# Performance work log

Hardware: AMD Instinct MI355X
Metric: run time of the kernel (lower is better)

The kernel has to match this reference:

```python
import jax, jax.numpy as jnp
import numpy as np

N_NODES = 50000
N_EDGES = 800000
IN_CH = 128
HID_CH = 128
OUT_CH = 10
NUM_GRAPHS = 128


def setup_inputs() -> dict:
    key = jax.random.key(0)
    ks = jax.random.split(key, 10)
    x = jax.random.normal(ks[0], (N_NODES, IN_CH), dtype=jnp.float32)
    edge_index = jax.random.randint(ks[1], (2, N_EDGES), 0, N_NODES, dtype=jnp.int64)
    batch = jnp.sort(jax.random.randint(ks[2], (N_NODES,), 0, NUM_GRAPHS, dtype=jnp.int64))
    s1 = 1.0 / np.sqrt(IN_CH)
    s2 = 1.0 / np.sqrt(HID_CH)
    W1 = jax.random.uniform(ks[3], (IN_CH, HID_CH), jnp.float32, -s1, s1)
    b1 = jnp.zeros((HID_CH,), jnp.float32)
    W2 = jax.random.uniform(ks[4], (HID_CH, HID_CH), jnp.float32, -s2, s2)
    b2 = jnp.zeros((HID_CH,), jnp.float32)
    Wc = jax.random.uniform(ks[5], (HID_CH, OUT_CH), jnp.float32, -s2, s2)
    bc = jax.random.uniform(ks[6], (OUT_CH,), jnp.float32, -s2, s2)
    return {"x": x, "edge_index": edge_index, "batch": batch,
            "W1": W1, "b1": b1, "W2": W2, "b2": b2, "Wc": Wc, "bc": bc}


def _gcn_norm(edge_index, num_nodes):
    # add self-loops, compute symmetric normalization deg^-1/2[src]*deg^-1/2[dst]
    loop = jnp.arange(num_nodes, dtype=edge_index.dtype)
    src = jnp.concatenate([edge_index[0], loop])
    dst = jnp.concatenate([edge_index[1], loop])
    deg = jax.ops.segment_sum(jnp.ones_like(dst, dtype=jnp.float32), dst,
                              num_segments=num_nodes)
    dinv = jnp.where(deg > 0, jax.lax.rsqrt(deg), 0.0)
    norm = dinv[src] * dinv[dst]
    return src, dst, norm


def _gcn_conv(h, src, dst, norm, W, b, num_nodes):
    h = h @ W                                    # [N, out]
    msg = h[src] * norm[:, None]                 # [E+N, out] gather + scale
    agg = jax.ops.segment_sum(msg, dst, num_segments=num_nodes)
    return agg + b


def reference(x, edge_index, batch, W1, b1, W2, b2, Wc, bc):
    n = x.shape[0]
    src, dst, norm = _gcn_norm(edge_index, n)
    h = jax.nn.relu(_gcn_conv(x, src, dst, norm, W1, b1, n))
    h = jax.nn.relu(_gcn_conv(h, src, dst, norm, W2, b2, n))
    # global mean pool over graphs
    sums = jax.ops.segment_sum(h, batch, num_segments=NUM_GRAPHS)
    cnts = jax.ops.segment_sum(jnp.ones((n,), jnp.float32), batch,
                               num_segments=NUM_GRAPHS)
    pooled = sums / jnp.maximum(cnts, 1.0)[:, None]
    # dropout is identity in eval mode
    return pooled @ Wc + bc
```

## Files before the change

### kernel.cpp

```cpp
#include <hip/hip_runtime.h>

#define N_NODES 50000
#define N_EDGES 800000
#define CH 128
#define NOUT 10
#define NUM_GRAPHS 128
#define POOL_CHUNK 50
#define GR 64
#define GEMM_BLOCKS ((N_NODES + GR - 1) / GR)
#define FILL_SEGS 128
#define FILL_CHUNK (N_EDGES / FILL_SEGS)
#define DST_RANGE (N_NODES / 8)
#define DEG_CAP 64

typedef __attribute__((ext_vector_type(8))) short bf16x8;
typedef __attribute__((ext_vector_type(4))) float f32x4;

union FragU { uint4 u; bf16x8 s; };

__device__ __forceinline__ unsigned pack_bf16(float a, float b) {
    unsigned ua = __float_as_uint(a), ub = __float_as_uint(b);
    ua += 0x7fffu + ((ua >> 16) & 1u);
    ub += 0x7fffu + ((ub >> 16) & 1u);
    return (ua >> 16) | (ub & 0xffff0000u);
}

__device__ __forceinline__ unsigned short cvt_bf16(float v) {
    unsigned u = __float_as_uint(v);
    u += 0x7fffu + ((u >> 16) & 1u);
    return (unsigned short)(u >> 16);
}

__global__ __launch_bounds__(256) void k_prep(const float* __restrict__ W1,
                                              const float* __restrict__ W2,
                                              unsigned short* __restrict__ Wb1,
                                              unsigned short* __restrict__ Wb2,
                                              int* __restrict__ fill_pos,
                                              float* __restrict__ psum) {
    if (blockIdx.x < 2) {
        const float* W = blockIdx.x ? W2 : W1;
        unsigned short* Wb = blockIdx.x ? Wb2 : Wb1;
        for (int i = threadIdx.x; i < CH * CH; i += 256) {
            int k = i >> 7, n = i & 127;
            Wb[((((k >> 3) << 7) + n) << 3) + (k & 7)] = cvt_bf16(W[i]);
        }
    } else if (blockIdx.x < 198) {
        int idx = (blockIdx.x - 2) * 256 + threadIdx.x;
        if (idx < N_NODES) fill_pos[idx] = 0;
    } else {
        psum[(blockIdx.x - 198) * 256 + threadIdx.x] = 0.f;
    }
}

template <bool SCALE>
__device__ __forceinline__ void gemm_body9(const float* __restrict__ X,
                                           const unsigned short* __restrict__ Wb,
                                           unsigned short* __restrict__ Yb,
                                           const int* __restrict__ cnt,
                                           int bid) {
    const int tid = threadIdx.x;
    const int w = tid >> 6;
    const int lane = tid & 63;
    const int m = lane & 15;
    const int quad = lane >> 4;
    const int row0 = bid * GR + w * 16;

    int row_a = row0 + m;
    if (row_a > N_NODES - 1) row_a = N_NODES - 1;
    const float4* Xr = (const float4*)(X + (size_t)row_a * CH) + quad * 2;

    f32x4 acc[8];
    #pragma unroll
    for (int ct = 0; ct < 8; ++ct) acc[ct] = (f32x4){0.f, 0.f, 0.f, 0.f};

    const uint4* Wq = (const uint4*)Wb;
    #pragma unroll
    for (int ks = 0; ks < 4; ++ks) {
        float4 a0 = Xr[ks * 8];
        float4 a1 = Xr[ks * 8 + 1];
        FragU af;
        af.u.x = pack_bf16(a0.x, a0.y);
        af.u.y = pack_bf16(a0.z, a0.w);
        af.u.z = pack_bf16(a1.x, a1.y);
        af.u.w = pack_bf16(a1.z, a1.w);
        const int kg = ks * 4 + quad;
        #pragma unroll
        for (int ct = 0; ct < 8; ++ct) {
            FragU bfu;
            bfu.u = Wq[kg * 128 + ct * 16 + m];
            acc[ct] = __builtin_amdgcn_mfma_f32_16x16x32_bf16(af.s, bfu.s, acc[ct], 0, 0, 0);
        }
    }

    #pragma unroll
    for (int r = 0; r < 4; ++r) {
        int row = row0 + quad * 4 + r;
        if (row < N_NODES) {
            float dv = SCALE ? rsqrtf((float)(cnt[row] + 1)) : 1.0f;
            unsigned short* yrow = Yb + (size_t)row * CH + m;
            #pragma unroll
            for (int ct = 0; ct < 8; ++ct)
                yrow[ct * 16] = cvt_bf16(SCALE ? acc[ct][r] * dv : acc[ct][r]);
        }
    }
}

__global__ __launch_bounds__(256) void k_gemm_fill(const float* __restrict__ X,
                                                   const unsigned short* __restrict__ Wb,
                                                   unsigned short* __restrict__ Yb,
                                                   const int* __restrict__ src,
                                                   const int* __restrict__ dst,
                                                   int* __restrict__ fill_pos,
                                                   int* __restrict__ csr_src) {
    if (blockIdx.x < GEMM_BLOCKS) {
        gemm_body9<false>(X, Wb, Yb, nullptr, blockIdx.x);
    } else {
        const int b = blockIdx.x - GEMM_BLOCKS;
        const int rng = b & 7;
        const int seg = b >> 3;
        const int lo = rng * DST_RANGE, hi = lo + DST_RANGE;
        const int base = seg * FILL_CHUNK;
        for (int it = 0; it < FILL_CHUNK; it += 256) {
            int e = base + it + threadIdx.x;
            if (it + (int)threadIdx.x < FILL_CHUNK) {
                int d = dst[e];
                if (d >= lo && d < hi) {
                    int slot = atomicAdd(&fill_pos[d], 1);
                    if (slot < DEG_CAP) csr_src[(d << 6) + slot] = src[e];
                }
            }
        }
    }
}

__global__ __launch_bounds__(256) void k_gemm9b(const float* __restrict__ X,
                                                const unsigned short* __restrict__ Wb,
                                                unsigned short* __restrict__ Yb,
                                                const int* __restrict__ cnt) {
    gemm_body9<true>(X, Wb, Yb, cnt, blockIdx.x);
}

__global__ __launch_bounds__(256) void k_gather1(const unsigned* __restrict__ tb,
                                                 const int* __restrict__ csr_src,
                                                 const int* __restrict__ cnt,
                                                 const float* __restrict__ b,
                                                 float* __restrict__ h) {
    const int wid = threadIdx.x >> 6;
    const int lane = threadIdx.x & 63;
    const int v = blockIdx.x * 4 + wid;

    int len = cnt[v];
    const float dv = rsqrtf((float)(len + 1));
    if (len > DEG_CAP) len = DEG_CAP;

    float x0 = 0.f, y0 = 0.f, x1 = 0.f, y1 = 0.f;
    float x2 = 0.f, y2 = 0.f, x3 = 0.f, y3 = 0.f;

    int u_l = 0;
    float w_l = 0.f;
    if (lane < len) {
        u_l = csr_src[(v << 6) + lane];
        w_l = rsqrtf((float)(cnt[u_l] + 1));
    }
    int j = 0;
    for (; j + 3 < len; j += 4) {
        int u0 = __shfl(u_l, j),     u1 = __shfl(u_l, j + 1);
        int u2 = __shfl(u_l, j + 2), u3 = __shfl(u_l, j + 3);
        float w0 = __shfl(w_l, j),     w1 = __shfl(w_l, j + 1);
        float w2 = __shfl(w_l, j + 2), w3 = __shfl(w_l, j + 3);
        unsigned r0 = tb[(size_t)u0 * 64 + lane];
        unsigned r1 = tb[(size_t)u1 * 64 + lane];
        unsigned r2 = tb[(size_t)u2 * 64 + lane];
        unsigned r3 = tb[(size_t)u3 * 64 + lane];
        x0 = fmaf(w0, __uint_as_float(r0 << 16), x0);
        y0 = fmaf(w0, __uint_as_float(r0 & 0xffff0000u), y0);
        x1 = fmaf(w1, __uint_as_float(r1 << 16), x1);
        y1 = fmaf(w1, __uint_as_float(r1 & 0xffff0000u), y1);
        x2 = fmaf(w2, __uint_as_float(r2 << 16), x2);
        y2 = fmaf(w2, __uint_as_float(r2 & 0xffff0000u), y2);
        x3 = fmaf(w3, __uint_as_float(r3 << 16), x3);
        y3 = fmaf(w3, __uint_as_float(r3 & 0xffff0000u), y3);
    }
    for (; j < len; ++j) {
        int u = __shfl(u_l, j);
        float w = __shfl(w_l, j);
        unsigned r = tb[(size_t)u * 64 + lane];
        x0 = fmaf(w, __uint_as_float(r << 16), x0);
        y0 = fmaf(w, __uint_as_float(r & 0xffff0000u), y0);
    }

    unsigned rs = tb[(size_t)v * 64 + lane];
    float sx = x0 + x1 + x2 + x3 + dv * __uint_as_float(rs << 16);
    float sy = y0 + y1 + y2 + y3 + dv * __uint_as_float(rs & 0xffff0000u);
    float2 bb = ((const float2*)b)[lane];
    float2 o;
    o.x = fmaxf(fmaf(dv, sx, bb.x), 0.f);
    o.y = fmaxf(fmaf(dv, sy, bb.y), 0.f);
    ((float2*)h)[(size_t)v * 64 + lane] = o;
}

__global__ __launch_bounds__(256) void k_gather2(const unsigned* __restrict__ tb,
                                                 const int* __restrict__ csr_src,
                                                 const int* __restrict__ cnt,
                                                 const float* __restrict__ b,
                                                 float* __restrict__ h) {
    const int wid = threadIdx.x >> 6;
    const int lane = threadIdx.x & 63;
    const int v = blockIdx.x * 4 + wid;

    int len = cnt[v];
    const float dv = rsqrtf((float)(len + 1));
    if (len > DEG_CAP) len = DEG_CAP;

    float x0 = 0.f, y0 = 0.f, x1 = 0.f, y1 = 0.f;
    float x2 = 0.f, y2 = 0.f, x3 = 0.f, y3 = 0.f;

    int u_l = 0;
    if (lane < len) u_l = csr_src[(v << 6) + lane];
    int j = 0;
    for (; j + 3 < len; j += 4) {
        int u0 = __shfl(u_l, j),     u1 = __shfl(u_l, j + 1);
        int u2 = __shfl(u_l, j + 2), u3 = __shfl(u_l, j + 3);
        unsigned r0 = tb[(size_t)u0 * 64 + lane];
        unsigned r1 = tb[(size_t)u1 * 64 + lane];
        unsigned r2 = tb[(size_t)u2 * 64 + lane];
        unsigned r3 = tb[(size_t)u3 * 64 + lane];
        x0 += __uint_as_float(r0 << 16); y0 += __uint_as_float(r0 & 0xffff0000u);
        x1 += __uint_as_float(r1 << 16); y1 += __uint_as_float(r1 & 0xffff0000u);
        x2 += __uint_as_float(r2 << 16); y2 += __uint_as_float(r2 & 0xffff0000u);
        x3 += __uint_as_float(r3 << 16); y3 += __uint_as_float(r3 & 0xffff0000u);
    }
    for (; j < len; ++j) {
        int u = __shfl(u_l, j);
        unsigned r = tb[(size_t)u * 64 + lane];
        x0 += __uint_as_float(r << 16); y0 += __uint_as_float(r & 0xffff0000u);
    }

    unsigned rs = tb[(size_t)v * 64 + lane];
    float sx = x0 + x1 + x2 + x3 + __uint_as_float(rs << 16);
    float sy = y0 + y1 + y2 + y3 + __uint_as_float(rs & 0xffff0000u);
    float2 bb = ((const float2*)b)[lane];
    float2 o;
    o.x = fmaxf(fmaf(dv, sx, bb.x), 0.f);
    o.y = fmaxf(fmaf(dv, sy, bb.y), 0.f);
    ((float2*)h)[(size_t)v * 64 + lane] = o;
}

__global__ __launch_bounds__(128) void k_pool2(const float* __restrict__ h,
                                               const int* __restrict__ batch,
                                               float* __restrict__ psum) {
    const int c = threadIdx.x;
    const int v0 = blockIdx.x * POOL_CHUNK;
    __shared__ int bg[POOL_CHUNK];
    if (c < POOL_CHUNK) bg[c] = batch[v0 + c];
    __syncthreads();

    float acc = 0.f;
    int g = bg[0];
    #pragma unroll 5
    for (int j = 0; j < POOL_CHUNK; ++j) {
        int bgj = bg[j];
        float val = h[(size_t)(v0 + j) * CH + c];
        if (bgj != g) {
            atomicAdd(&psum[g * CH + c], acc);
            acc = 0.f;
            g = bgj;
        }
        acc += val;
    }
    atomicAdd(&psum[g * CH + c], acc);
}

__global__ __launch_bounds__(128) void k_classify(const float* __restrict__ psum,
                                                  const int* __restrict__ batch,
                                                  const float* __restrict__ Wc,
                                                  const float* __restrict__ bc,
                                                  float* __restrict__ out) {
    __shared__ float p[CH];
    __shared__ float sinv;
    int g = blockIdx.x;
    int tid = threadIdx.x;
    if (tid == 0) {
        int lo = 0, hi = N_NODES;
        while (lo < hi) { int mid = (lo + hi) >> 1; if (batch[mid] < g) lo = mid + 1; else hi = mid; }
        int start = lo;
        lo = 0; hi = N_NODES;
        while (lo < hi) { int mid = (lo + hi) >> 1; if (batch[mid] < g + 1) lo = mid + 1; else hi = mid; }
        sinv = 1.0f / fmaxf((float)(lo - start), 1.0f);
    }
    __syncthreads();
    p[tid] = psum[g * CH + tid] * sinv;
    __syncthreads();
    if (tid < NOUT) {
        float acc = bc[tid];
        #pragma unroll 4
        for (int k = 0; k < CH; ++k) acc += p[k] * Wc[k * NOUT + tid];
        out[g * NOUT + tid] = acc;
    }
}

extern "C" void kernel_launch(void* const* d_in, const int* in_sizes, int n_in,
                              void* d_out, int out_size, void* d_ws, size_t ws_size,
                              hipStream_t stream) {
    const float* x     = (const float*)d_in[0];
    const int*   ei    = (const int*)d_in[1];
    const int*   batch = (const int*)d_in[2];
    const float* W1    = (const float*)d_in[3];
    const float* b1    = (const float*)d_in[4];
    const float* W2    = (const float*)d_in[5];
    const float* b2    = (const float*)d_in[6];
    const float* Wc    = (const float*)d_in[7];
    const float* bc    = (const float*)d_in[8];
    float* out = (float*)d_out;

    const int* src = ei;
    const int* dst = ei + N_EDGES;

    int*            fill_pos = (int*)d_ws;
    int*            csr_src  = fill_pos + N_NODES;
    unsigned short* wb1      = (unsigned short*)(csr_src + (size_t)N_NODES * DEG_CAP);
    unsigned short* wb2      = wb1 + CH * CH;
    unsigned short* tb       = wb2 + CH * CH;
    float*          hbuf     = (float*)(tb + (size_t)N_NODES * CH);
    float*          psum     = hbuf + (size_t)N_NODES * CH;

    k_prep<<<198 + 64, 256, 0, stream>>>(W1, W2, wb1, wb2, fill_pos, psum);

    k_gemm_fill<<<GEMM_BLOCKS + FILL_SEGS * 8, 256, 0, stream>>>(
        x, wb1, tb, src, dst, fill_pos, csr_src);

    k_gather1<<<N_NODES / 4, 256, 0, stream>>>((unsigned*)tb, csr_src, fill_pos, b1, hbuf);

    k_gemm9b<<<GEMM_BLOCKS, 256, 0, stream>>>(hbuf, wb2, tb, fill_pos);

    k_gather2<<<N_NODES / 4, 256, 0, stream>>>((unsigned*)tb, csr_src, fill_pos, b2, hbuf);

    k_pool2<<<N_NODES / POOL_CHUNK, 128, 0, stream>>>(hbuf, batch, psum);
    k_classify<<<NUM_GRAPHS, 128, 0, stream>>>(psum, batch, Wc, bc, out);
}
```

Measured before the change: 260.8 us.

## Bin edges by destination range before CSR fill in a separate kernel

Result: no change. 262.1 us (+0.5%).

```diff
diff --git a/kernel.cpp b/kernel.cpp
--- a/kernel.cpp
+++ b/kernel.cpp
@@ -105,31 +105,49 @@
     }
 }
 
-__global__ __launch_bounds__(256) void k_gemm_fill(const float* __restrict__ X,
-                                                   const unsigned short* __restrict__ Wb,
-                                                   unsigned short* __restrict__ Yb,
-                                                   const int* __restrict__ src,
-                                                   const int* __restrict__ dst,
-                                                   int* __restrict__ fill_pos,
-                                                   int* __restrict__ csr_src) {
+__global__ __launch_bounds__(256) void k_gemm_bin(const float* __restrict__ X,
+                                                  const unsigned short* __restrict__ Wb,
+                                                  unsigned short* __restrict__ Yb,
+                                                  const int* __restrict__ src,
+                                                  const int* __restrict__ dst,
+                                                  int2* __restrict__ bins,
+                                                  int* __restrict__ bin_cnt) {
     if (blockIdx.x < GEMM_BLOCKS) {
         gemm_body9<false>(X, Wb, Yb, nullptr, blockIdx.x);
     } else {
-        const int b = blockIdx.x - GEMM_BLOCKS;
-        const int rng = b & 7;
-        const int seg = b >> 3;
-        const int lo = rng * DST_RANGE, hi = lo + DST_RANGE;
-        const int base = seg * FILL_CHUNK;
+        __shared__ int cur[8];
+        if (threadIdx.x < 8) cur[threadIdx.x] = 0;
+        __syncthreads();
+        const int s = blockIdx.x - GEMM_BLOCKS;
+        const int base = s * FILL_CHUNK;
         for (int it = 0; it < FILL_CHUNK; it += 256) {
-            int e = base + it + threadIdx.x;
-            if (it + (int)threadIdx.x < FILL_CHUNK) {
+            int i = it + threadIdx.x;
+            if (i < FILL_CHUNK) {
+                int e = base + i;
                 int d = dst[e];
-                if (d >= lo && d < hi) {
-                    int slot = atomicAdd(&fill_pos[d], 1);
-                    if (slot < DEG_CAP) csr_src[(d << 6) + slot] = src[e];
-                }
+                int sr = src[e];
+                int r = (unsigned)d / DST_RANGE;
+                int slot = atomicAdd(&cur[r], 1);
+                bins[((size_t)s * 8 + r) * FILL_CHUNK + slot] = make_int2(d, sr);
             }
         }
+        __syncthreads();
+        if (threadIdx.x < 8) bin_cnt[s * 8 + threadIdx.x] = cur[threadIdx.x];
+    }
+}
+
+__global__ __launch_bounds__(256) void k_fill_b(const int2* __restrict__ bins,
+                                                const int* __restrict__ bin_cnt,
+                                                int* __restrict__ fill_pos,
+                                                int* __restrict__ csr_src) {
+    const int r = blockIdx.x & 7;
+    const int s = blockIdx.x >> 3;
+    const int c = bin_cnt[s * 8 + r];
+    const int2* bin = &bins[((size_t)s * 8 + r) * FILL_CHUNK];
+    for (int i = threadIdx.x; i < c; i += 256) {
+        int2 p = bin[i];
+        int slot = atomicAdd(&fill_pos[p.x], 1);
+        if (slot < DEG_CAP) csr_src[(p.x << 6) + slot] = p.y;
     }
 }
 
@@ -323,11 +341,15 @@
     unsigned short* tb       = wb2 + CH * CH;
     float*          hbuf     = (float*)(tb + (size_t)N_NODES * CH);
     float*          psum     = hbuf + (size_t)N_NODES * CH;
+    int*            bin_cnt  = (int*)(psum + NUM_GRAPHS * CH);
+    int2*           bins     = (int2*)(bin_cnt + 1024);
 
     k_prep<<<198 + 64, 256, 0, stream>>>(W1, W2, wb1, wb2, fill_pos, psum);
 
-    k_gemm_fill<<<GEMM_BLOCKS + FILL_SEGS * 8, 256, 0, stream>>>(
-        x, wb1, tb, src, dst, fill_pos, csr_src);
+    k_gemm_bin<<<GEMM_BLOCKS + FILL_SEGS, 256, 0, stream>>>(
+        x, wb1, tb, src, dst, bins, bin_cnt);
+
+    k_fill_b<<<FILL_SEGS * 8, 256, 0, stream>>>(bins, bin_cnt, fill_pos, csr_src);
 
     k_gather1<<<N_NODES / 4, 256, 0, stream>>>((unsigned*)tb, csr_src, fill_pos, b1, hbuf);
 
```
